# Performance work log

Measured on AMD Instinct MI355X. Metric: run time of the kernel, lower is better.

Reference implementation:

```python
import jax, jax.numpy as jnp
import numpy as np

HID = 256


def setup_inputs() -> dict:
    key0 = jax.random.key(0)
    ks = jax.random.split(key0, 6)
    bsz, m, Lq, Lk = 8, 16, 64, 2048
    query = jax.random.normal(ks[0], (bsz, Lq, HID), dtype=jnp.float32)
    key = jax.random.normal(ks[1], (bsz * m, Lk, HID), dtype=jnp.float32)
    # nn.Linear params (weight is [out, in]); init scale ~ 1/sqrt(fan_in)
    s = 1.0 / np.sqrt(HID)
    w_q = jax.random.uniform(ks[2], (HID, HID), jnp.float32, -s, s)
    b_q = jax.random.uniform(ks[3], (HID,), jnp.float32, -s, s)
    w_k = jax.random.uniform(ks[4], (HID, HID), jnp.float32, -s, s)
    b_k = jax.random.uniform(ks[5], (HID,), jnp.float32, -s, s)
    return {"query": query, "key": key, "w_q": w_q, "b_q": b_q, "w_k": w_k, "b_k": b_k}


def reference(query, key, w_q, b_q, w_k, b_k):
    bsz = query.shape[0]
    msz = key.shape[0]
    m = msz // bsz
    hid = query.shape[-1]
    scale = jnp.sqrt(jnp.float32(hid))
    Q = jnp.einsum("bqh,oh->bqo", query, w_q) + b_q            # [b, Lq, h]
    K = jnp.einsum("nkh,oh->nko", key, w_k) + b_k              # [b*m, Lk, h]
    K = K.reshape(bsz, m, -1, hid)                               # [b, m, Lk, h]
    key_r = key.reshape(bsz, m, -1, hid)                         # [b, m, Lk, h]
    # energy[b,m,q,k] = Q[b,q,:] . K[b,m,k,:] / sqrt(hid)
    energy = jnp.einsum("bqh,bmkh->bmqk", Q, K) / scale         # [b, m, Lq, Lk]
    total_attention = jnp.sum(energy, axis=-2)                   # [b, m, Lk]
    attention = jnp.mean(total_attention, axis=-1)               # [b, m]
    max_index = jnp.argmax(attention, axis=-1)                   # [b]
    # gather the raw key block for the best candidate per batch item
    val = jnp.take_along_axis(key_r, max_index[:, None, None, None], axis=1)
    return val[:, 0]                                             # [b, Lk, h]
```

## Files before the change

kernel.cpp:

```cpp
#include <hip/hip_runtime.h>

#define HID 256
#define LK  2048
#define LQ  64
#define BSZ 8
#define M   16
#define NKEY (BSZ * M)
#define SPLIT 8

__global__ void colsum_kernel(const float* __restrict__ query,
                              const float* __restrict__ key,
                              const float* __restrict__ w_q,
                              const float* __restrict__ b_q,
                              const float* __restrict__ w_k,
                              float* __restrict__ partial,
                              float* __restrict__ u,
                              unsigned long long* __restrict__ amax) {
    const int bid  = blockIdx.x;
    const int t    = threadIdx.x;
    const int wave = t >> 6;
    const int lane = t & 63;

    if (bid < BSZ) {
        if (t == 0) amax[bid] = 0ull;
        __shared__ float lds[4][HID];
        __shared__ float qs[HID];
        __shared__ float qsv[HID];
        const int b = bid;
        const float* qbase = query + (size_t)b * LQ * HID;

        float4 a = make_float4(0.f, 0.f, 0.f, 0.f);
#pragma unroll
        for (int r = 0; r < LQ / 4; ++r) {
            float4 v = ((const float4*)(qbase + (size_t)(wave * (LQ / 4) + r) * HID))[lane];
            a.x += v.x; a.y += v.y; a.z += v.z; a.w += v.w;
        }
        ((float4*)lds[wave])[lane] = a;
        __syncthreads();
        qs[t] = (lds[0][t] + lds[1][t]) + (lds[2][t] + lds[3][t]);
        __syncthreads();

        const float4* wrow = (const float4*)(w_q + (size_t)t * HID);
        float acc = 0.f;
#pragma unroll
        for (int h4 = 0; h4 < HID / 4; ++h4) {
            float4 w = wrow[h4];
            acc += w.x * qs[h4 * 4 + 0] + w.y * qs[h4 * 4 + 1]
                 + w.z * qs[h4 * 4 + 2] + w.w * qs[h4 * 4 + 3];
        }
        qsv[t] = acc + (float)LQ * b_q[t];
        __syncthreads();

        float4 ua = make_float4(0.f, 0.f, 0.f, 0.f);
#pragma unroll 8
        for (int i = 0; i < 64; ++i) {
            const int o = wave * 64 + i;
            float4 w = ((const float4*)(w_k + (size_t)o * HID))[lane];
            const float q = qsv[o];
            ua.x += q * w.x; ua.y += q * w.y; ua.z += q * w.z; ua.w += q * w.w;
        }
        ((float4*)lds[wave])[lane] = ua;
        __syncthreads();
        u[(size_t)b * HID + t] = (lds[0][t] + lds[1][t]) + (lds[2][t] + lds[3][t]);
    } else {
        const int kb    = bid - BSZ;
        const int n     = kb / SPLIT;
        const int chunk = kb % SPLIT;
        const int rows  = LK / SPLIT;
        const float* base = key + (size_t)n * LK * HID + (size_t)chunk * rows * HID;

        const int rpw = rows / 4;
        const int r0  = wave * rpw;
        float4 a0 = make_float4(0.f, 0.f, 0.f, 0.f);
        float4 a1 = make_float4(0.f, 0.f, 0.f, 0.f);
        float4 a2 = make_float4(0.f, 0.f, 0.f, 0.f);
        float4 a3 = make_float4(0.f, 0.f, 0.f, 0.f);
#pragma unroll 4
        for (int i = 0; i < rpw; i += 4) {
            float4 v0 = ((const float4*)(base + (size_t)(r0 + i + 0) * HID))[lane];
            float4 v1 = ((const float4*)(base + (size_t)(r0 + i + 1) * HID))[lane];
            float4 v2 = ((const float4*)(base + (size_t)(r0 + i + 2) * HID))[lane];
            float4 v3 = ((const float4*)(base + (size_t)(r0 + i + 3) * HID))[lane];
            a0.x += v0.x; a0.y += v0.y; a0.z += v0.z; a0.w += v0.w;
            a1.x += v1.x; a1.y += v1.y; a1.z += v1.z; a1.w += v1.w;
            a2.x += v2.x; a2.y += v2.y; a2.z += v2.z; a2.w += v2.w;
            a3.x += v3.x; a3.y += v3.y; a3.z += v3.z; a3.w += v3.w;
        }
        a0.x = (a0.x + a1.x) + (a2.x + a3.x);
        a0.y = (a0.y + a1.y) + (a2.y + a3.y);
        a0.z = (a0.z + a1.z) + (a2.z + a3.z);
        a0.w = (a0.w + a1.w) + (a2.w + a3.w);

        __shared__ float klds[4][HID];
        ((float4*)klds[wave])[lane] = a0;
        __syncthreads();
        partial[(size_t)kb * HID + t] =
            (klds[0][t] + klds[1][t]) + (klds[2][t] + klds[3][t]);
    }
}

__global__ void att_kernel(const float* __restrict__ partial,
                           const float* __restrict__ u,
                           unsigned long long* __restrict__ amax) {
    const int n    = blockIdx.x;
    const int b    = n / M;
    const int m    = n % M;
    const int t    = threadIdx.x;
    const int wave = t >> 6;
    const int lane = t & 63;

    const float* p = partial + (size_t)n * SPLIT * HID + t;
    float s = 0.f;
    float sv[SPLIT];
#pragma unroll
    for (int c = 0; c < SPLIT; ++c) sv[c] = p[(size_t)c * HID];
#pragma unroll
    for (int c = 0; c < SPLIT; ++c) s += sv[c];

    float v = s * u[(size_t)b * HID + t];
    for (int off = 32; off; off >>= 1) v += __shfl_down(v, off);

    __shared__ float wp[4];
    if (lane == 0) wp[wave] = v;
    __syncthreads();
    if (t == 0) {
        float att = (wp[0] + wp[1]) + (wp[2] + wp[3]);
        unsigned int fb = __float_as_uint(att);
        unsigned int mono = (fb & 0x80000000u) ? ~fb : (fb | 0x80000000u);
        unsigned long long pack =
            ((unsigned long long)mono << 32) | (unsigned int)(M - 1 - m);
        atomicMax(&amax[b], pack);
    }
}

__global__ void gather_kernel(const float* __restrict__ key,
                              const unsigned long long* __restrict__ amax,
                              float* __restrict__ out) {
    const int b = blockIdx.y;
    const unsigned long long v = amax[b];
    const int m = M - 1 - (int)(v & 0xFFFFFFFFu);
    const int n = b * M + m;
    const size_t per_b = (size_t)LK * HID / 4;
    const size_t off = (size_t)blockIdx.x * blockDim.x + threadIdx.x;
    ((float4*)out)[(size_t)b * per_b + off] =
        ((const float4*)key)[(size_t)n * per_b + off];
}

extern "C" void kernel_launch(void* const* d_in, const int* in_sizes, int n_in,
                              void* d_out, int out_size, void* d_ws, size_t ws_size,
                              hipStream_t stream) {
    const float* query = (const float*)d_in[0];
    const float* key   = (const float*)d_in[1];
    const float* w_q   = (const float*)d_in[2];
    const float* b_q   = (const float*)d_in[3];
    const float* w_k   = (const float*)d_in[4];
    float* out = (float*)d_out;

    unsigned long long* amax = (unsigned long long*)d_ws;
    float* partial = (float*)(amax + BSZ);
    float* u       = partial + (size_t)NKEY * SPLIT * HID;

    hipLaunchKernelGGL(colsum_kernel, dim3(BSZ + NKEY * SPLIT), dim3(256), 0,
                       stream, query, key, w_q, b_q, w_k, partial, u, amax);

    hipLaunchKernelGGL(att_kernel, dim3(NKEY), dim3(256), 0, stream,
                       partial, u, amax);

    hipLaunchKernelGGL(gather_kernel, dim3(512, BSZ), dim3(256), 0, stream,
                       key, amax, out);
}
```

Baseline: 74.72 us.

## Fuse colsum, attention and gather into one cooperative persistent kernel

Replaces the three-kernel pipeline with a single cooperative grid kernel. Each block column-sums key chunks into registers, the last blocks compute the projected query vector u, and after a grid sync the blocks reduce dot products into att with atomics. After a second grid sync every block does the argmax itself and gathers the chosen key rows. This removes the extra launches and the partial-sum round trip through memory, at the cost of two grid-wide barriers and occupancy-dependent grid sizing. The three-kernel path stays as a fallback and moves to a finer split of the key rows.

```diff
diff --git a/kernel.cpp b/kernel.cpp
--- a/kernel.cpp
+++ b/kernel.cpp
@@ -1,4 +1,7 @@
 #include <hip/hip_runtime.h>
+#include <hip/hip_cooperative_groups.h>
+
+namespace cg = cooperative_groups;
 
 #define HID 256
 #define LK  2048
@@ -6,7 +9,149 @@
 #define BSZ 8
 #define M   16
 #define NKEY (BSZ * M)
-#define SPLIT 8
+#define SPLIT 32
+#define CHUNKS (NKEY * SPLIT)
+#define ROWS (LK / SPLIT)
+#define RPW (ROWS / 4)
+#define MAXC 4
+
+__global__ __launch_bounds__(256)
+void fused_kernel(const float* __restrict__ query,
+                  const float* __restrict__ key,
+                  const float* __restrict__ w_q,
+                  const float* __restrict__ b_q,
+                  const float* __restrict__ w_k,
+                  float* __restrict__ u,
+                  float* __restrict__ att,
+                  float* __restrict__ out,
+                  int nb) {
+    cg::grid_group grid = cg::this_grid();
+    const int bid  = blockIdx.x;
+    const int t    = threadIdx.x;
+    const int wave = t >> 6;
+    const int lane = t & 63;
+
+    __shared__ float lds[4][HID];
+    __shared__ float wp[4];
+
+    if (bid == 0 && t < NKEY) att[t] = 0.f;
+
+    float csum[MAXC];
+    int   ccid[MAXC];
+    int   nc = 0;
+    for (int c = bid; c < CHUNKS; c += nb) {
+        const int n  = c >> 5;
+        const int ch = c & (SPLIT - 1);
+        const float* base = key + (size_t)n * LK * HID + (size_t)ch * ROWS * HID;
+        const int r0 = wave * RPW;
+
+        float4 a0 = make_float4(0.f, 0.f, 0.f, 0.f);
+        float4 a1 = make_float4(0.f, 0.f, 0.f, 0.f);
+        float4 a2 = make_float4(0.f, 0.f, 0.f, 0.f);
+        float4 a3 = make_float4(0.f, 0.f, 0.f, 0.f);
+#pragma unroll 4
+        for (int i = 0; i < RPW; i += 4) {
+            float4 v0 = ((const float4*)(base + (size_t)(r0 + i + 0) * HID))[lane];
+            float4 v1 = ((const float4*)(base + (size_t)(r0 + i + 1) * HID))[lane];
+            float4 v2 = ((const float4*)(base + (size_t)(r0 + i + 2) * HID))[lane];
+            float4 v3 = ((const float4*)(base + (size_t)(r0 + i + 3) * HID))[lane];
+            a0.x += v0.x; a0.y += v0.y; a0.z += v0.z; a0.w += v0.w;
+            a1.x += v1.x; a1.y += v1.y; a1.z += v1.z; a1.w += v1.w;
+            a2.x += v2.x; a2.y += v2.y; a2.z += v2.z; a2.w += v2.w;
+            a3.x += v3.x; a3.y += v3.y; a3.z += v3.z; a3.w += v3.w;
+        }
+        a0.x = (a0.x + a1.x) + (a2.x + a3.x);
+        a0.y = (a0.y + a1.y) + (a2.y + a3.y);
+        a0.z = (a0.z + a1.z) + (a2.z + a3.z);
+        a0.w = (a0.w + a1.w) + (a2.w + a3.w);
+
+        ((float4*)lds[wave])[lane] = a0;
+        __syncthreads();
+        csum[nc] = (lds[0][t] + lds[1][t]) + (lds[2][t] + lds[3][t]);
+        ccid[nc] = c;
+        ++nc;
+        __syncthreads();
+    }
+
+    if (bid >= nb - BSZ) {
+        const int qb = bid - (nb - BSZ);
+        __shared__ float qs[HID];
+        __shared__ float qsv[HID];
+        const float* qbase = query + (size_t)qb * LQ * HID;
+
+        float4 a = make_float4(0.f, 0.f, 0.f, 0.f);
+#pragma unroll
+        for (int r = 0; r < LQ / 4; ++r) {
+            float4 v = ((const float4*)(qbase + (size_t)(wave * (LQ / 4) + r) * HID))[lane];
+            a.x += v.x; a.y += v.y; a.z += v.z; a.w += v.w;
+        }
+        ((float4*)lds[wave])[lane] = a;
+        __syncthreads();
+        qs[t] = (lds[0][t] + lds[1][t]) + (lds[2][t] + lds[3][t]);
+        __syncthreads();
+
+        const float4* wrow = (const float4*)(w_q + (size_t)t * HID);
+        float acc = 0.f;
+#pragma unroll
+        for (int h4 = 0; h4 < HID / 4; ++h4) {
+            float4 w = wrow[h4];
+            acc += w.x * qs[h4 * 4 + 0] + w.y * qs[h4 * 4 + 1]
+                 + w.z * qs[h4 * 4 + 2] + w.w * qs[h4 * 4 + 3];
+        }
+        qsv[t] = acc + (float)LQ * b_q[t];
+        __syncthreads();
+
+        float4 ua = make_float4(0.f, 0.f, 0.f, 0.f);
+#pragma unroll 8
+        for (int i = 0; i < 64; ++i) {
+            const int o = wave * 64 + i;
+            float4 w = ((const float4*)(w_k + (size_t)o * HID))[lane];
+            const float q = qsv[o];
+            ua.x += q * w.x; ua.y += q * w.y; ua.z += q * w.z; ua.w += q * w.w;
+        }
+        ((float4*)lds[wave])[lane] = ua;
+        __syncthreads();
+        u[(size_t)qb * HID + t] = (lds[0][t] + lds[1][t]) + (lds[2][t] + lds[3][t]);
+    }
+
+    grid.sync();
+
+    for (int i = 0; i < nc; ++i) {
+        const int n = ccid[i] >> 5;
+        const int b = n >> 4;
+        float v = csum[i] * u[(size_t)b * HID + t];
+        for (int off = 32; off; off >>= 1) v += __shfl_down(v, off);
+        if (lane == 0) wp[wave] = v;
+        __syncthreads();
+        if (t == 0) atomicAdd(&att[n], (wp[0] + wp[1]) + (wp[2] + wp[3]));
+        __syncthreads();
+    }
+
+    grid.sync();
+
+    __shared__ float satt[NKEY];
+    __shared__ int   sbest[BSZ];
+    if (t < NKEY) satt[t] = att[t];
+    __syncthreads();
+    if (t < BSZ) {
+        const float* a = satt + t * M;
+        int best = 0;
+        float bv = a[0];
+        for (int m = 1; m < M; ++m)
+            if (a[m] > bv) { bv = a[m]; best = m; }
+        sbest[t] = best;
+    }
+    __syncthreads();
+
+    const size_t total = (size_t)BSZ * LK * HID / 4;
+    for (size_t i = (size_t)bid * blockDim.x + t; i < total;
+         i += (size_t)nb * blockDim.x) {
+        const int b = (int)(i >> 17);
+        const size_t off = i & (size_t)131071;
+        const size_t n = (size_t)(b * M + sbest[b]);
+        ((float4*)out)[i] = ((const float4*)key)[(n << 17) | off];
+    }
+}
 
 __global__ void colsum_kernel(const float* __restrict__ query,
                               const float* __restrict__ key,
@@ -23,26 +168,16 @@
 
     if (bid < BSZ) {
         if (t == 0) amax[bid] = 0ull;
-        __shared__ float lds[4][HID];
         __shared__ float qs[HID];
         __shared__ float qsv[HID];
-        const int b = bid;
-        const float* qbase = query + (size_t)b * LQ * HID;
-
-        float4 a = make_float4(0.f, 0.f, 0.f, 0.f);
-#pragma unroll
-        for (int r = 0; r < LQ / 4; ++r) {
-            float4 v = ((const float4*)(qbase + (size_t)(wave * (LQ / 4) + r) * HID))[lane];
-            a.x += v.x; a.y += v.y; a.z += v.z; a.w += v.w;
-        }
-        ((float4*)lds[wave])[lane] = a;
-        __syncthreads();
-        qs[t] = (lds[0][t] + lds[1][t]) + (lds[2][t] + lds[3][t]);
-        __syncthreads();
-
+        const float* qbase = query + (size_t)bid * LQ * HID;
+        float s = 0.f;
+        for (int r = 0; r < LQ; ++r) s += qbase[(size_t)r * HID + t];
+        qs[t] = s;
+        __syncthreads();
         const float4* wrow = (const float4*)(w_q + (size_t)t * HID);
         float acc = 0.f;
-#pragma unroll
+#pragma unroll 8
         for (int h4 = 0; h4 < HID / 4; ++h4) {
             float4 w = wrow[h4];
             acc += w.x * qs[h4 * 4 + 0] + w.y * qs[h4 * 4 + 1]
@@ -50,33 +185,22 @@
         }
         qsv[t] = acc + (float)LQ * b_q[t];
         __syncthreads();
-
-        float4 ua = make_float4(0.f, 0.f, 0.f, 0.f);
-#pragma unroll 8
-        for (int i = 0; i < 64; ++i) {
-            const int o = wave * 64 + i;
-            float4 w = ((const float4*)(w_k + (size_t)o * HID))[lane];
-            const float q = qsv[o];
-            ua.x += q * w.x; ua.y += q * w.y; ua.z += q * w.z; ua.w += q * w.w;
-        }
-        ((float4*)lds[wave])[lane] = ua;
-        __syncthreads();
-        u[(size_t)b * HID + t] = (lds[0][t] + lds[1][t]) + (lds[2][t] + lds[3][t]);
+        float uh = 0.f;
+#pragma unroll 4
+        for (int o = 0; o < HID; ++o) uh += qsv[o] * w_k[(size_t)o * HID + t];
+        u[(size_t)bid * HID + t] = uh;
     } else {
-        const int kb    = bid - BSZ;
-        const int n     = kb / SPLIT;
-        const int chunk = kb % SPLIT;
-        const int rows  = LK / SPLIT;
-        const float* base = key + (size_t)n * LK * HID + (size_t)chunk * rows * HID;
-
-        const int rpw = rows / 4;
-        const int r0  = wave * rpw;
+        const int kb = bid - BSZ;
+        const int n  = kb >> 5;
+        const int ch = kb & (SPLIT - 1);
+        const float* base = key + (size_t)n * LK * HID + (size_t)ch * ROWS * HID;
+        const int r0 = wave * RPW;
         float4 a0 = make_float4(0.f, 0.f, 0.f, 0.f);
         float4 a1 = make_float4(0.f, 0.f, 0.f, 0.f);
         float4 a2 = make_float4(0.f, 0.f, 0.f, 0.f);
         float4 a3 = make_float4(0.f, 0.f, 0.f, 0.f);
 #pragma unroll 4
-        for (int i = 0; i < rpw; i += 4) {
+        for (int i = 0; i < RPW; i += 4) {
             float4 v0 = ((const float4*)(base + (size_t)(r0 + i + 0) * HID))[lane];
             float4 v1 = ((const float4*)(base + (size_t)(r0 + i + 1) * HID))[lane];
             float4 v2 = ((const float4*)(base + (size_t)(r0 + i + 2) * HID))[lane];
@@ -90,7 +214,6 @@
         a0.y = (a0.y + a1.y) + (a2.y + a3.y);
         a0.z = (a0.z + a1.z) + (a2.z + a3.z);
         a0.w = (a0.w + a1.w) + (a2.w + a3.w);
-
         __shared__ float klds[4][HID];
         ((float4*)klds[wave])[lane] = a0;
         __syncthreads();
@@ -103,23 +226,23 @@
                            const float* __restrict__ u,
                            unsigned long long* __restrict__ amax) {
     const int n    = blockIdx.x;
-    const int b    = n / M;
-    const int m    = n % M;
+    const int b    = n >> 4;
+    const int m    = n & (M - 1);
     const int t    = threadIdx.x;
     const int wave = t >> 6;
     const int lane = t & 63;
 
     const float* p = partial + (size_t)n * SPLIT * HID + t;
-    float s = 0.f;
-    float sv[SPLIT];
+    float s0 = 0.f, s1 = 0.f, s2 = 0.f, s3 = 0.f;
 #pragma unroll
-    for (int c = 0; c < SPLIT; ++c) sv[c] = p[(size_t)c * HID];
-#pragma unroll
-    for (int c = 0; c < SPLIT; ++c) s += sv[c];
-
-    float v = s * u[(size_t)b * HID + t];
+    for (int c = 0; c < SPLIT; c += 4) {
+        s0 += p[(size_t)(c + 0) * HID];
+        s1 += p[(size_t)(c + 1) * HID];
+        s2 += p[(size_t)(c + 2) * HID];
+        s3 += p[(size_t)(c + 3) * HID];
+    }
+    float v = ((s0 + s1) + (s2 + s3)) * u[(size_t)b * HID + t];
     for (int off = 32; off; off >>= 1) v += __shfl_down(v, off);
-
     __shared__ float wp[4];
     if (lane == 0) wp[wave] = v;
     __syncthreads();
@@ -157,15 +280,41 @@
     float* out = (float*)d_out;
 
     unsigned long long* amax = (unsigned long long*)d_ws;
-    float* partial = (float*)(amax + BSZ);
-    float* u       = partial + (size_t)NKEY * SPLIT * HID;
-
-    hipLaunchKernelGGL(colsum_kernel, dim3(BSZ + NKEY * SPLIT), dim3(256), 0,
-                       stream, query, key, w_q, b_q, w_k, partial, u, amax);
-
-    hipLaunchKernelGGL(att_kernel, dim3(NKEY), dim3(256), 0, stream,
-                       partial, u, amax);
-
-    hipLaunchKernelGGL(gather_kernel, dim3(512, BSZ), dim3(256), 0, stream,
-                       key, amax, out);
-}
+    float* att     = (float*)(amax + BSZ);
+    float* u       = att + NKEY;
+    float* partial = u + (size_t)BSZ * HID;
+
+    int coop = 0;
+    hipDeviceGetAttribute(&coop, hipDeviceAttributeCooperativeLaunch, 0);
+
+    bool launched = false;
+    if (coop) {
+        int maxActive = 0;
+        hipError_t oe = hipOccupancyMaxActiveBlocksPerMultiprocessor(
+            &maxActive, (const void*)fused_kernel, 256, 0);
+        int ncu = 0;
+        hipDeviceGetAttribute(&ncu, hipDeviceAttributeMultiprocessorCount, 0);
+        if (oe == hipSuccess && maxActive >= 1 && ncu >= 1) {
+            long long cap = (long long)ncu * maxActive;
+            int nb = (int)(cap > 2056 ? 2056 : cap);
+            if (nb >= 1024 + BSZ) {
+                void* args[] = {(void*)&query, (void*)&key, (void*)&w_q,
+                                (void*)&b_q,   (void*)&w_k, (void*)&u,
+                                (void*)&att,   (void*)&out, (void*)&nb};
+                hipError_t le = hipLaunchCooperativeKernel(
+                    (const void*)fused_kernel, dim3(nb), dim3(256), args, 0,
+                    stream);
+                launched = (le == hipSuccess);
+            }
+        }
+    }
+
+    if (!launched) {
+        hipLaunchKernelGGL(colsum_kernel, dim3(BSZ + CHUNKS), dim3(256), 0,
+                           stream, query, key, w_q, b_q, w_k, partial, u, amax);
+        hipLaunchKernelGGL(att_kernel, dim3(NKEY), dim3(256), 0, stream,
+                           partial, u, amax);
+        hipLaunchKernelGGL(gather_kernel, dim3(512, BSZ), dim3(256), 0, stream,
+                           key, amax, out);
+    }
+}
```

Result: faster. 69.11 us (-7.5%).
